# Kernel tuning notes

Measured on AMD Instinct MI355X. Metric: run time of the kernel, lower is better.

Reference implementation:

```python
import jax, jax.numpy as jnp
import numpy as np

E = 32        # num_local_experts
TOP_K = 4     # num_experts_per_tok
H = 1024      # hidden_size
I = 1024      # intermediate_size (expert_dim)
ALPHA = 1.702
LIMIT = 7.0
B, S = 2, 1024


def setup_inputs() -> dict:
    key = jax.random.key(0)
    ks = jax.random.split(key, 8)
    scale = 0.02
    return {
        "hidden_states": jax.random.normal(ks[0], (B, S, H), dtype=jnp.float32),
        "gate_up_proj": jax.random.normal(ks[1], (E, H, 2 * I), dtype=jnp.float32) * scale,
        "gate_up_proj_bias": jax.random.normal(ks[2], (E, 2 * I), dtype=jnp.float32) * scale,
        "down_proj": jax.random.normal(ks[3], (E, I, H), dtype=jnp.float32) * scale,
        "down_proj_bias": jax.random.normal(ks[4], (E, H), dtype=jnp.float32) * scale,
        "router_weight": jax.random.normal(ks[5], (E, H), dtype=jnp.float32) * scale,
        "router_bias": jax.random.normal(ks[6], (E,), dtype=jnp.float32) * scale,
    }


def reference(hidden_states, gate_up_proj, gate_up_proj_bias, down_proj,
              down_proj_bias, router_weight, router_bias):
    b, s, h = hidden_states.shape
    x = hidden_states.reshape(-1, h)                       # [T, H], T = B*S
    t = x.shape[0]

    # ---- router: linear -> topk -> softmax over topk -> scatter to dense scores
    router_logits = x @ router_weight.T + router_bias      # [T, E]
    top_vals, top_idx = jax.lax.top_k(router_logits, TOP_K)
    top_w = jax.nn.softmax(top_vals, axis=-1)
    router_scores = jnp.zeros_like(router_logits).at[
        jnp.arange(t)[:, None], top_idx].set(top_w)        # [T, E]

    # ---- experts (dense all-expert path, interleaved gate/up columns)
    gate_w = gate_up_proj[..., 0::2]                       # [E, H, I]
    up_w = gate_up_proj[..., 1::2]                         # [E, H, I]
    gate_b = gate_up_proj_bias[..., 0::2]                  # [E, I]
    up_b = gate_up_proj_bias[..., 1::2]                    # [E, I]

    gate = jnp.einsum('th,ehi->eti', x, gate_w) + gate_b[:, None, :]
    up = jnp.einsum('th,ehi->eti', x, up_w) + up_b[:, None, :]
    gate = jnp.minimum(gate, LIMIT)
    up = jnp.clip(up, -LIMIT, LIMIT)
    glu = gate * jax.nn.sigmoid(gate * ALPHA)
    next_states = jnp.einsum('eti,eih->eth', (up + 1.0) * glu, down_proj)
    next_states = next_states + down_proj_bias[:, None, :]  # [E, T, H]

    # ---- combine: weight each expert output by its routing score and sum
    routed = jnp.einsum('eth,te->th', next_states, router_scores)
    return routed.reshape(b, s, h), router_scores
```

## Files before the change

kernel.cpp:

```cpp
#include <hip/hip_runtime.h>
#include <cstdint>
#include <cstddef>

#define E_ 32
#define TOPK_ 4
#define H_ 1024
#define I_ 1024
#define T_ 2048
#define ALPHA_ 1.702f
#define LIMIT_ 7.0f
#define BK_ 32
#define BKP_ 40
#define TP_ 66

typedef __attribute__((ext_vector_type(8))) short s8;
typedef __attribute__((ext_vector_type(4))) float f4;

__device__ __forceinline__ unsigned short f2bf(float f) {
  unsigned int u = __float_as_uint(f);
  return (unsigned short)((u + 0x7fffu + ((u >> 16) & 1u)) >> 16);
}

__global__ __launch_bounds__(256)
void cast_x_kernel(const float* __restrict__ x, unsigned short* __restrict__ xb) {
  size_t i = (size_t)(blockIdx.x * 256 + threadIdx.x) * 8;
  float4 a = *(const float4*)(x + i);
  float4 b = *(const float4*)(x + i + 4);
  s8 v;
  v[0] = (short)f2bf(a.x); v[1] = (short)f2bf(a.y);
  v[2] = (short)f2bf(a.z); v[3] = (short)f2bf(a.w);
  v[4] = (short)f2bf(b.x); v[5] = (short)f2bf(b.y);
  v[6] = (short)f2bf(b.z); v[7] = (short)f2bf(b.w);
  *(s8*)(xb + i) = v;
}

__global__ __launch_bounds__(256)
void transpose_cast(const float* __restrict__ src, unsigned short* __restrict__ dst,
                    int src_rows, int src_cols, int deint) {
  int e = blockIdx.z;
  int c0 = blockIdx.x * 64;
  int r0 = blockIdx.y * 64;
  int tid = threadIdx.x;
  __shared__ unsigned short ldsT[64][TP_];

  const float* sp = src + (size_t)e * src_rows * src_cols
                        + (size_t)r0 * src_cols + c0;
  int r = tid >> 2, cq = tid & 3;
  const float* rowp = sp + (size_t)r * src_cols + cq * 4;
  #pragma unroll
  for (int j = 0; j < 4; ++j) {
    float4 v = *(const float4*)(rowp + j * 16);
    int c = cq * 4 + j * 16;
    ldsT[c + 0][r] = f2bf(v.x);
    ldsT[c + 1][r] = f2bf(v.y);
    ldsT[c + 2][r] = f2bf(v.z);
    ldsT[c + 3][r] = f2bf(v.w);
  }
  __syncthreads();

  int co = tid >> 2, hq = tid & 3;
  s8 v0 = *(s8*)&ldsT[co][hq * 16];
  s8 v1 = *(s8*)&ldsT[co][hq * 16 + 8];
  int C = c0 + co;
  size_t out_off;
  if (deint) {
    out_off = (size_t)e * src_cols * src_rows
            + (size_t)(C & 1) * (src_cols >> 1) * src_rows
            + (size_t)(C >> 1) * src_rows + r0 + hq * 16;
  } else {
    out_off = (size_t)e * src_cols * src_rows
            + (size_t)C * src_rows + r0 + hq * 16;
  }
  *(s8*)(dst + out_off) = v0;
  *(s8*)(dst + out_off + 8) = v1;
}

__global__ __launch_bounds__(128)
void router_kernel(const float* __restrict__ x,
                   const float* __restrict__ rw,
                   const float* __restrict__ rb,
                   float* __restrict__ scores,
                   int* __restrict__ counts,
                   int* __restrict__ tok_list,
                   float* __restrict__ w_list) {
  int t = blockIdx.x;
  int tid = threadIdx.x;
  __shared__ float partial[128];
  __shared__ float logits[E_];
  int e = tid & 31, q = tid >> 5;
  const float4* xp = (const float4*)(x + (size_t)t * H_ + q * 256);
  const float4* wp = (const float4*)(rw + (size_t)e * H_ + q * 256);
  float s = 0.f;
  #pragma unroll 8
  for (int h = 0; h < 64; ++h) {
    float4 a = xp[h], b = wp[h];
    s += a.x * b.x + a.y * b.y + a.z * b.z + a.w * b.w;
  }
  partial[tid] = s;
  __syncthreads();
  if (tid < 32)
    logits[tid] = partial[tid] + partial[tid + 32] + partial[tid + 64] +
                  partial[tid + 96] + rb[tid];
  __syncthreads();
  if (tid == 0) {
    float l[E_];
    #pragma unroll
    for (int i = 0; i < E_; ++i) l[i] = logits[i];
    int idx[TOPK_]; float v[TOPK_];
    for (int k = 0; k < TOPK_; ++k) {
      int bi = 0; float bv = -1e30f;
      for (int i = 0; i < E_; ++i)
        if (l[i] > bv) { bv = l[i]; bi = i; }
      idx[k] = bi; v[k] = bv; l[bi] = -1e30f;
    }
    float m = v[0], den = 0.f, w[TOPK_];
    for (int k = 0; k < TOPK_; ++k) { w[k] = expf(v[k] - m); den += w[k]; }
    float inv = 1.f / den;
    float* srow = scores + (size_t)t * E_;
    #pragma unroll
    for (int i = 0; i < E_; ++i) srow[i] = 0.f;
    for (int k = 0; k < TOPK_; ++k) {
      float wk = w[k] * inv;
      srow[idx[k]] = wk;
      int pos = atomicAdd(&counts[idx[k]], 1);
      tok_list[idx[k] * T_ + pos] = t * TOPK_ + k;
      w_list[idx[k] * T_ + pos] = wk;
    }
  }
}

__global__ __launch_bounds__(256)
void gateup_mfma(const unsigned short* __restrict__ xb,
                 const unsigned short* __restrict__ wgu,
                 const float* __restrict__ gb,
                 const int* __restrict__ counts,
                 const int* __restrict__ tok_list,
                 unsigned short* __restrict__ act) {
  int e = blockIdx.z;
  int cnt = counts[e];
  int t0 = blockIdx.y * 256;
  if (t0 >= cnt) return;
  int itile = blockIdx.x;
  int tid = threadIdx.x;
  int lane = tid & 63;
  int wave = tid >> 6;

  __shared__ __align__(16) unsigned short Xs[2][256][BKP_];
  __shared__ __align__(16) unsigned short Wg[2][128][BKP_];
  __shared__ int toks[256];

  {
    int slot = t0 + tid;
    toks[tid] = (slot < cnt) ? tok_list[e * T_ + slot] : -1;
  }
  __syncthreads();

  f4 acc[4][8] = {};

  int srow = tid >> 2;
  int koq  = (tid & 3) * 8;
  int aenc[4];
  const unsigned short* axp[4];
  #pragma unroll
  for (int p = 0; p < 4; ++p) {
    aenc[p] = toks[srow + p * 64];
    axp[p] = xb + (size_t)(aenc[p] >> 2) * H_ + koq;
  }
  const unsigned short* bp0 = wgu + (size_t)e * 2 * I_ * H_
                            + (size_t)(itile * 64 + srow) * H_ + koq;
  const unsigned short* bp1 = bp0 + (size_t)I_ * H_;

  int fm = lane & 15, ko = (lane >> 4) * 8;

  s8 pA[4];
  s8 pB[2];
  #pragma unroll
  for (int p = 0; p < 4; ++p) {
    s8 z = {};
    pA[p] = (aenc[p] >= 0) ? *(const s8*)(axp[p]) : z;
  }
  pB[0] = *(const s8*)bp0;
  pB[1] = *(const s8*)bp1;

  int buf = 0;
  for (int c = 0; c < H_ / BK_; ++c) {
    #pragma unroll
    for (int p = 0; p < 4; ++p) *(s8*)&Xs[buf][srow + p * 64][koq] = pA[p];
    *(s8*)&Wg[buf][srow][koq] = pB[0];
    *(s8*)&Wg[buf][64 + srow][koq] = pB[1];
    __syncthreads();
    if (c + 1 < H_ / BK_) {
      int k0 = (c + 1) * BK_;
      #pragma unroll
      for (int p = 0; p < 4; ++p)
        if (aenc[p] >= 0) pA[p] = *(const s8*)(axp[p] + k0);
      pB[0] = *(const s8*)(bp0 + k0);
      pB[1] = *(const s8*)(bp1 + k0);
    }
    {
      s8 a[4];
      #pragma unroll
      for (int f = 0; f < 4; ++f)
        a[f] = *(s8*)&Xs[buf][wave * 64 + f * 16 + fm][ko];
      #pragma unroll
      for (int g = 0; g < 8; ++g) {
        s8 b = *(s8*)&Wg[buf][g * 16 + fm][ko];
        #pragma unroll
        for (int f = 0; f < 4; ++f)
          acc[f][g] = __builtin_amdgcn_mfma_f32_16x16x32_bf16(a[f], b, acc[f][g], 0, 0, 0);
      }
    }
    buf ^= 1;
  }

  int rq = lane >> 4;
  #pragma unroll
  for (int gg = 0; gg < 4; ++gg) {
    int i = itile * 64 + gg * 16 + fm;
    float bg_ = gb[e * 2 * I_ + 2 * i];
    float bu_ = gb[e * 2 * I_ + 2 * i + 1];
    #pragma unroll
    for (int f = 0; f < 4; ++f) {
      #pragma unroll
      for (int r = 0; r < 4; ++r) {
        int m = wave * 64 + f * 16 + rq * 4 + r;
        int enc = toks[m];
        if (enc < 0) continue;
        float gv = acc[f][gg][r] + bg_;
        float uv = acc[f][gg + 4][r] + bu_;
        gv = fminf(gv, LIMIT_);
        uv = fminf(fmaxf(uv, -LIMIT_), LIMIT_);
        float glu = gv / (1.f + __expf(-ALPHA_ * gv));
        act[(size_t)enc * I_ + i] = f2bf((uv + 1.f) * glu);
      }
    }
  }
}

__global__ __launch_bounds__(256)
void down_mfma(const unsigned short* __restrict__ act,
               const unsigned short* __restrict__ wdt,
               const float* __restrict__ db,
               const int* __restrict__ counts,
               const int* __restrict__ tok_list,
               const float* __restrict__ w_list,
               float* __restrict__ dsout) {
  int e = blockIdx.z;
  int cnt = counts[e];
  int t0 = blockIdx.y * 256;
  if (t0 >= cnt) return;
  int htile = blockIdx.x;
  int tid = threadIdx.x;
  int lane = tid & 63;
  int wave = tid >> 6;

  __shared__ __align__(16) unsigned short Xs[2][256][BKP_];
  __shared__ __align__(16) unsigned short Wd[2][128][BKP_];
  __shared__ int toks[256];
  __shared__ float tws[256];

  {
    int slot = t0 + tid;
    bool ok = slot < cnt;
    toks[tid] = ok ? tok_list[e * T_ + slot] : -1;
    tws[tid]  = ok ? w_list[e * T_ + slot] : 0.f;
  }
  __syncthreads();

  f4 acc[4][8] = {};

  int srow = tid >> 2;
  int koq  = (tid & 3) * 8;
  int aenc[4];
  const unsigned short* axp[4];
  #pragma unroll
  for (int p = 0; p < 4; ++p) {
    aenc[p] = toks[srow + p * 64];
    axp[p] = act + (size_t)aenc[p] * I_ + koq;
  }
  const unsigned short* bp0 = wdt + (size_t)e * H_ * I_
                            + (size_t)(htile * 128 + srow) * I_ + koq;
  const unsigned short* bp1 = bp0 + (size_t)64 * I_;

  int fm = lane & 15, ko = (lane >> 4) * 8;

  s8 pA[4];
  s8 pB[2];
  #pragma unroll
  for (int p = 0; p < 4; ++p) {
    s8 z = {};
    pA[p] = (aenc[p] >= 0) ? *(const s8*)(axp[p]) : z;
  }
  pB[0] = *(const s8*)bp0;
  pB[1] = *(const s8*)bp1;

  int buf = 0;
  for (int c = 0; c < I_ / BK_; ++c) {
    #pragma unroll
    for (int p = 0; p < 4; ++p) *(s8*)&Xs[buf][srow + p * 64][koq] = pA[p];
    *(s8*)&Wd[buf][srow][koq] = pB[0];
    *(s8*)&Wd[buf][64 + srow][koq] = pB[1];
    __syncthreads();
    if (c + 1 < I_ / BK_) {
      int k0 = (c + 1) * BK_;
      #pragma unroll
      for (int p = 0; p < 4; ++p)
        if (aenc[p] >= 0) pA[p] = *(const s8*)(axp[p] + k0);
      pB[0] = *(const s8*)(bp0 + k0);
      pB[1] = *(const s8*)(bp1 + k0);
    }
    {
      s8 a[4];
      #pragma unroll
      for (int f = 0; f < 4; ++f)
        a[f] = *(s8*)&Xs[buf][wave * 64 + f * 16 + fm][ko];
      #pragma unroll
      for (int g = 0; g < 8; ++g) {
        s8 b = *(s8*)&Wd[buf][g * 16 + fm][ko];
        #pragma unroll
        for (int f = 0; f < 4; ++f)
          acc[f][g] = __builtin_amdgcn_mfma_f32_16x16x32_bf16(a[f], b, acc[f][g], 0, 0, 0);
      }
    }
    buf ^= 1;
  }

  int rq = lane >> 4;
  #pragma unroll
  for (int g = 0; g < 8; ++g) {
    int h = htile * 128 + g * 16 + fm;
    float bias = db[e * H_ + h];
    #pragma unroll
    for (int f = 0; f < 4; ++f) {
      #pragma unroll
      for (int r = 0; r < 4; ++r) {
        int m = wave * 64 + f * 16 + rq * 4 + r;
        int enc = toks[m];
        if (enc < 0) continue;
        dsout[(size_t)enc * H_ + h] = (acc[f][g][r] + bias) * tws[m];
      }
    }
  }
}

__global__ __launch_bounds__(256)
void combine_kernel(const float* __restrict__ dsout,
                    float* __restrict__ routed) {
  int idx = blockIdx.x * 256 + threadIdx.x;
  int t = idx >> 8;
  int h = (idx & 255) * 4;
  const float* base = dsout + (size_t)t * 4 * H_ + h;
  float4 a = *(const float4*)(base);
  float4 b = *(const float4*)(base + H_);
  float4 c = *(const float4*)(base + 2 * H_);
  float4 d = *(const float4*)(base + 3 * H_);
  float4 o;
  o.x = a.x + b.x + c.x + d.x;
  o.y = a.y + b.y + c.y + d.y;
  o.z = a.z + b.z + c.z + d.z;
  o.w = a.w + b.w + c.w + d.w;
  *(float4*)(routed + (size_t)t * H_ + h) = o;
}

extern "C" void kernel_launch(void* const* d_in, const int* in_sizes, int n_in,
                              void* d_out, int out_size, void* d_ws, size_t ws_size,
                              hipStream_t stream) {
  (void)in_sizes; (void)n_in; (void)out_size; (void)ws_size;
  const float* x    = (const float*)d_in[0];
  const float* gup  = (const float*)d_in[1];
  const float* gupb = (const float*)d_in[2];
  const float* dwn  = (const float*)d_in[3];
  const float* dwnb = (const float*)d_in[4];
  const float* rw   = (const float*)d_in[5];
  const float* rb   = (const float*)d_in[6];

  float* routed = (float*)d_out;
  float* scores = (float*)d_out + (size_t)T_ * H_;

  char* ws = (char*)d_ws;
  int*   counts   = (int*)ws;
  int*   tok_list = (int*)(ws + ((size_t)1 << 20));
  float* w_list   = (float*)(ws + ((size_t)1 << 20) + (size_t)E_ * T_ * 4);
  unsigned short* xbf = (unsigned short*)(ws + ((size_t)2 << 20));
  unsigned short* act = (unsigned short*)(ws + ((size_t)8 << 20));
  unsigned short* wgu_b = (unsigned short*)(ws + ((size_t)24 << 20));
  float*          dsout = (float*)(ws + ((size_t)24 << 20));
  unsigned short* wdt_b = (unsigned short*)(ws + ((size_t)24 << 20)
                                            + (size_t)E_ * 2 * I_ * H_ * 2);

  hipMemsetAsync(counts, 0, E_ * sizeof(int), stream);

  cast_x_kernel<<<(T_ * H_ / 8) / 256, 256, 0, stream>>>(x, xbf);
  transpose_cast<<<dim3(2 * I_ / 64, H_ / 64, E_), 256, 0, stream>>>(
      gup, wgu_b, H_, 2 * I_, 1);
  transpose_cast<<<dim3(H_ / 64, I_ / 64, E_), 256, 0, stream>>>(
      dwn, wdt_b, I_, H_, 0);
  router_kernel<<<T_, 128, 0, stream>>>(x, rw, rb, scores, counts, tok_list, w_list);
  gateup_mfma<<<dim3(16, 8, 32), 256, 0, stream>>>(xbf, wgu_b, gupb,
                                                   counts, tok_list, act);
  down_mfma<<<dim3(8, 8, 32), 256, 0, stream>>>(act, wdt_b, dwnb,
                                                counts, tok_list, w_list, dsout);
  combine_kernel<<<(T_ * H_ / 4) / 256, 256, 0, stream>>>(dsout, routed);
}
```

Baseline: 788.9 us.

## Load activation fragments directly to registers, widen K-step to 64 with swizzled LDS weights

The expert GEMMs now skip staging the token (A) tile in shared memory. Each wave reads its MFMA A fragments straight from global memory into double-buffered registers, and only the weight tile goes through a double-buffered LDS buffer. That buffer is widened to 64 along K and uses an XOR swizzle to avoid bank conflicts. The K loop runs in 16 steps of 64 instead of 32 steps of 32, which halves the barriers. Waves with no valid tokens skip their loads and MFMAs, and launch bounds request two blocks per CU. The trade-off is more register pressure and uncoalesced direct global reads of gathered rows, which may rely on cache hits.

```diff
diff --git a/kernel.cpp b/kernel.cpp
--- a/kernel.cpp
+++ b/kernel.cpp
@@ -9,8 +9,6 @@
 #define T_ 2048
 #define ALPHA_ 1.702f
 #define LIMIT_ 7.0f
-#define BK_ 32
-#define BKP_ 40
 #define TP_ 66
 
 typedef __attribute__((ext_vector_type(8))) short s8;
@@ -129,7 +127,50 @@
   }
 }
 
-__global__ __launch_bounds__(256)
+#define GEMM_STEP(P, ACUR, ANXT, SCUR, NSC)                                  \
+  {                                                                          \
+    *(s8*)&Wt[P][n0][wc0] = pB[0];                                           \
+    *(s8*)&Wt[P][n0][wc1] = pB[1];                                           \
+    *(s8*)&Wt[P][n0][wc2] = pB[2];                                           \
+    *(s8*)&Wt[P][n0][wc3] = pB[3];                                           \
+    __syncthreads();                                                         \
+    if ((SCUR) + 1 < (NSC)) {                                                \
+      const unsigned short* bq = bprow + ((SCUR) + 1) * 64 + half * 32;      \
+      pB[0] = *(const s8*)(bq);                                              \
+      pB[1] = *(const s8*)(bq + 8);                                          \
+      pB[2] = *(const s8*)(bq + 16);                                         \
+      pB[3] = *(const s8*)(bq + 24);                                         \
+      if (wactive) {                                                         \
+        _Pragma("unroll")                                                    \
+        for (int f = 0; f < 4; ++f) {                                        \
+          ANXT[f * 2]     = *(const s8*)(abase[f] + ((SCUR) + 1) * 64);      \
+          ANXT[f * 2 + 1] = *(const s8*)(abase[f] + ((SCUR) + 1) * 64 + 32); \
+        }                                                                    \
+      }                                                                      \
+    }                                                                        \
+    if (wactive) {                                                           \
+      const unsigned short* rb0 = &Wt[P][fm][rcol0];                         \
+      const unsigned short* rb1 = &Wt[P][fm][rcol1];                         \
+      _Pragma("unroll")                                                      \
+      for (int g = 0; g < 8; ++g) {                                          \
+        s8 b0 = *(const s8*)(rb0 + g * 1024);                                \
+        _Pragma("unroll")                                                    \
+        for (int f = 0; f < 4; ++f)                                          \
+          acc[f][g] = __builtin_amdgcn_mfma_f32_16x16x32_bf16(               \
+              ACUR[f * 2], b0, acc[f][g], 0, 0, 0);                          \
+      }                                                                      \
+      _Pragma("unroll")                                                      \
+      for (int g = 0; g < 8; ++g) {                                          \
+        s8 b1 = *(const s8*)(rb1 + g * 1024);                                \
+        _Pragma("unroll")                                                    \
+        for (int f = 0; f < 4; ++f)                                          \
+          acc[f][g] = __builtin_amdgcn_mfma_f32_16x16x32_bf16(               \
+              ACUR[f * 2 + 1], b1, acc[f][g], 0, 0, 0);                      \
+      }                                                                      \
+    }                                                                        \
+  }
+
+__global__ __launch_bounds__(256, 2)
 void gateup_mfma(const unsigned short* __restrict__ xb,
                  const unsigned short* __restrict__ wgu,
                  const float* __restrict__ gb,
@@ -145,8 +186,7 @@
   int lane = tid & 63;
   int wave = tid >> 6;
 
-  __shared__ __align__(16) unsigned short Xs[2][256][BKP_];
-  __shared__ __align__(16) unsigned short Wg[2][128][BKP_];
+  __shared__ __align__(16) unsigned short Wt[2][128][64];
   __shared__ int toks[256];
 
   {
@@ -155,62 +195,51 @@
   }
   __syncthreads();
 
+  bool wactive = (t0 + wave * 64) < cnt;
+  int fm = lane & 15, ko = (lane >> 4) * 8;
+
   f4 acc[4][8] = {};
 
-  int srow = tid >> 2;
-  int koq  = (tid & 3) * 8;
-  int aenc[4];
-  const unsigned short* axp[4];
+  const unsigned short* abase[4];
   #pragma unroll
-  for (int p = 0; p < 4; ++p) {
-    aenc[p] = toks[srow + p * 64];
-    axp[p] = xb + (size_t)(aenc[p] >> 2) * H_ + koq;
-  }
-  const unsigned short* bp0 = wgu + (size_t)e * 2 * I_ * H_
-                            + (size_t)(itile * 64 + srow) * H_ + koq;
-  const unsigned short* bp1 = bp0 + (size_t)I_ * H_;
-
-  int fm = lane & 15, ko = (lane >> 4) * 8;
-
-  s8 pA[4];
-  s8 pB[2];
-  #pragma unroll
-  for (int p = 0; p < 4; ++p) {
-    s8 z = {};
-    pA[p] = (aenc[p] >= 0) ? *(const s8*)(axp[p]) : z;
-  }
-  pB[0] = *(const s8*)bp0;
-  pB[1] = *(const s8*)bp1;
-
-  int buf = 0;
-  for (int c = 0; c < H_ / BK_; ++c) {
-    #pragma unroll
-    for (int p = 0; p < 4; ++p) *(s8*)&Xs[buf][srow + p * 64][koq] = pA[p];
-    *(s8*)&Wg[buf][srow][koq] = pB[0];
-    *(s8*)&Wg[buf][64 + srow][koq] = pB[1];
-    __syncthreads();
-    if (c + 1 < H_ / BK_) {
-      int k0 = (c + 1) * BK_;
+  for (int f = 0; f < 4; ++f) {
+    int enc = toks[wave * 64 + f * 16 + fm];
+    int row = (enc < 0) ? 0 : (enc >> 2);
+    abase[f] = xb + (size_t)row * H_ + ko;
+  }
+
+  int n0 = tid & 127, half = tid >> 7;
+  const unsigned short* bprow = wgu + (size_t)e * 2 * I_ * H_
+      + (size_t)((n0 < 64) ? (itile * 64 + n0) : (I_ + itile * 64 + (n0 - 64))) * H_;
+  int wsw = (n0 & 7) << 3;
+  int wc0 = (half * 32 + 0)  ^ wsw;
+  int wc1 = (half * 32 + 8)  ^ wsw;
+  int wc2 = (half * 32 + 16) ^ wsw;
+  int wc3 = (half * 32 + 24) ^ wsw;
+  int rsw = (fm & 7) << 3;
+  int rcol0 = (ko) ^ rsw;
+  int rcol1 = (32 + ko) ^ rsw;
+
+  s8 pB[4];
+  s8 aA[8], aB[8];
+  {
+    const unsigned short* bq = bprow + half * 32;
+    pB[0] = *(const s8*)(bq);
+    pB[1] = *(const s8*)(bq + 8);
+    pB[2] = *(const s8*)(bq + 16);
+    pB[3] = *(const s8*)(bq + 24);
+    if (wactive) {
       #pragma unroll
-      for (int p = 0; p < 4; ++p)
-        if (aenc[p] >= 0) pA[p] = *(const s8*)(axp[p] + k0);
-      pB[0] = *(const s8*)(bp0 + k0);
-      pB[1] = *(const s8*)(bp1 + k0);
-    }
-    {
-      s8 a[4];
-      #pragma unroll
-      for (int f = 0; f < 4; ++f)
-        a[f] = *(s8*)&Xs[buf][wave * 64 + f * 16 + fm][ko];
-      #pragma unroll
-      for (int g = 0; g < 8; ++g) {
-        s8 b = *(s8*)&Wg[buf][g * 16 + fm][ko];
-        #pragma unroll
-        for (int f = 0; f < 4; ++f)
-          acc[f][g] = __builtin_amdgcn_mfma_f32_16x16x32_bf16(a[f], b, acc[f][g], 0, 0, 0);
+      for (int f = 0; f < 4; ++f) {
+        aA[f * 2]     = *(const s8*)(abase[f]);
+        aA[f * 2 + 1] = *(const s8*)(abase[f] + 32);
       }
     }
-    buf ^= 1;
+  }
+
+  for (int s = 0; s < 16; s += 2) {
+    GEMM_STEP(0, aA, aB, s, 16)
+    GEMM_STEP(1, aB, aA, s + 1, 16)
   }
 
   int rq = lane >> 4;
@@ -237,7 +266,7 @@
   }
 }
 
-__global__ __launch_bounds__(256)
+__global__ __launch_bounds__(256, 2)
 void down_mfma(const unsigned short* __restrict__ act,
                const unsigned short* __restrict__ wdt,
                const float* __restrict__ db,
@@ -254,8 +283,7 @@
   int lane = tid & 63;
   int wave = tid >> 6;
 
-  __shared__ __align__(16) unsigned short Xs[2][256][BKP_];
-  __shared__ __align__(16) unsigned short Wd[2][128][BKP_];
+  __shared__ __align__(16) unsigned short Wt[2][128][64];
   __shared__ int toks[256];
   __shared__ float tws[256];
 
@@ -267,62 +295,51 @@
   }
   __syncthreads();
 
+  bool wactive = (t0 + wave * 64) < cnt;
+  int fm = lane & 15, ko = (lane >> 4) * 8;
+
   f4 acc[4][8] = {};
 
-  int srow = tid >> 2;
-  int koq  = (tid & 3) * 8;
-  int aenc[4];
-  const unsigned short* axp[4];
+  const unsigned short* abase[4];
   #pragma unroll
-  for (int p = 0; p < 4; ++p) {
-    aenc[p] = toks[srow + p * 64];
-    axp[p] = act + (size_t)aenc[p] * I_ + koq;
-  }
-  const unsigned short* bp0 = wdt + (size_t)e * H_ * I_
-                            + (size_t)(htile * 128 + srow) * I_ + koq;
-  const unsigned short* bp1 = bp0 + (size_t)64 * I_;
-
-  int fm = lane & 15, ko = (lane >> 4) * 8;
-
-  s8 pA[4];
-  s8 pB[2];
-  #pragma unroll
-  for (int p = 0; p < 4; ++p) {
-    s8 z = {};
-    pA[p] = (aenc[p] >= 0) ? *(const s8*)(axp[p]) : z;
-  }
-  pB[0] = *(const s8*)bp0;
-  pB[1] = *(const s8*)bp1;
-
-  int buf = 0;
-  for (int c = 0; c < I_ / BK_; ++c) {
-    #pragma unroll
-    for (int p = 0; p < 4; ++p) *(s8*)&Xs[buf][srow + p * 64][koq] = pA[p];
-    *(s8*)&Wd[buf][srow][koq] = pB[0];
-    *(s8*)&Wd[buf][64 + srow][koq] = pB[1];
-    __syncthreads();
-    if (c + 1 < I_ / BK_) {
-      int k0 = (c + 1) * BK_;
+  for (int f = 0; f < 4; ++f) {
+    int enc = toks[wave * 64 + f * 16 + fm];
+    int row = (enc < 0) ? 0 : enc;
+    abase[f] = act + (size_t)row * I_ + ko;
+  }
+
+  int n0 = tid & 127, half = tid >> 7;
+  const unsigned short* bprow = wdt + (size_t)e * H_ * I_
+      + (size_t)(htile * 128 + n0) * I_;
+  int wsw = (n0 & 7) << 3;
+  int wc0 = (half * 32 + 0)  ^ wsw;
+  int wc1 = (half * 32 + 8)  ^ wsw;
+  int wc2 = (half * 32 + 16) ^ wsw;
+  int wc3 = (half * 32 + 24) ^ wsw;
+  int rsw = (fm & 7) << 3;
+  int rcol0 = (ko) ^ rsw;
+  int rcol1 = (32 + ko) ^ rsw;
+
+  s8 pB[4];
+  s8 aA[8], aB[8];
+  {
+    const unsigned short* bq = bprow + half * 32;
+    pB[0] = *(const s8*)(bq);
+    pB[1] = *(const s8*)(bq + 8);
+    pB[2] = *(const s8*)(bq + 16);
+    pB[3] = *(const s8*)(bq + 24);
+    if (wactive) {
       #pragma unroll
-      for (int p = 0; p < 4; ++p)
-        if (aenc[p] >= 0) pA[p] = *(const s8*)(axp[p] + k0);
-      pB[0] = *(const s8*)(bp0 + k0);
-      pB[1] = *(const s8*)(bp1 + k0);
-    }
-    {
-      s8 a[4];
-      #pragma unroll
-      for (int f = 0; f < 4; ++f)
-        a[f] = *(s8*)&Xs[buf][wave * 64 + f * 16 + fm][ko];
-      #pragma unroll
-      for (int g = 0; g < 8; ++g) {
-        s8 b = *(s8*)&Wd[buf][g * 16 + fm][ko];
-        #pragma unroll
-        for (int f = 0; f < 4; ++f)
-          acc[f][g] = __builtin_amdgcn_mfma_f32_16x16x32_bf16(a[f], b, acc[f][g], 0, 0, 0);
+      for (int f = 0; f < 4; ++f) {
+        aA[f * 2]     = *(const s8*)(abase[f]);
+        aA[f * 2 + 1] = *(const s8*)(abase[f] + 32);
       }
     }
-    buf ^= 1;
+  }
+
+  for (int s = 0; s < 16; s += 2) {
+    GEMM_STEP(0, aA, aB, s, 16)
+    GEMM_STEP(1, aB, aA, s + 1, 16)
   }
 
   int rq = lane >> 4;
```

Measured after the change: 834.3 us. 5.8% more time.
